# Kernel optimization log

Hardware: AMD Instinct MI355X
Metric: run time of the kernel (lower is better)

Reference implementation:

```python
import jax, jax.numpy as jnp
import numpy as np

N_NODES = 10000
N_EDGES = 200000
NODE_DIM = 128
EDGE_DIM = 16
CONV_DIM = 64
HEADS = 5
NEG_SLOPE = 0.2


def gatv2_layer(x, src, dst, edge_attr, Wl, bl, We, att, bias):
    # PyG GATv2Conv, share_weights=True, concat=False, add_self_loops=True, eval mode
    N = x.shape[0]
    H, C = att.shape
    xl = (x @ Wl + bl).reshape(N, H, C)  # [N,H,C]; x_r = x_l (share_weights)
    # self loops, edge_attr fill_value='mean' (mean of incoming edge_attr per node)
    deg = jax.ops.segment_sum(jnp.ones(dst.shape[0], x.dtype), dst, num_segments=N)
    loop_attr = jax.ops.segment_sum(edge_attr, dst, num_segments=N) / jnp.maximum(deg, 1.0)[:, None]
    loop = jnp.arange(N, dtype=src.dtype)
    src_f = jnp.concatenate([src, loop])
    dst_f = jnp.concatenate([dst, loop])
    ea = jnp.concatenate([edge_attr, loop_attr], axis=0)
    e_emb = (ea @ We).reshape(-1, H, C)  # [E+N,H,C]
    m = jax.nn.leaky_relu(xl[src_f] + xl[dst_f] + e_emb, NEG_SLOPE)
    score = jnp.einsum('ehc,hc->eh', m, att)  # [E+N,H]
    # per-destination softmax over incoming edges
    smax = jax.ops.segment_max(score, dst_f, num_segments=N)
    ex = jnp.exp(score - smax[dst_f])
    denom = jax.ops.segment_sum(ex, dst_f, num_segments=N)
    alpha = ex / denom[dst_f]
    out = jax.ops.segment_sum(alpha[:, :, None] * xl[src_f], dst_f, num_segments=N)
    return out.mean(axis=1) + bias  # concat=False -> mean over heads


def setup_inputs() -> dict:
    key = jax.random.key(0)
    ks = jax.random.split(key, 32)
    inp = {
        'x': jax.random.normal(ks[0], (N_NODES, NODE_DIM), jnp.float32),
        'edge_index': jax.random.randint(ks[1], (2, N_EDGES), 0, N_NODES, dtype=jnp.int32),
        'edge_attr': jax.random.normal(ks[2], (N_EDGES, EDGE_DIM), jnp.float32),
    }
    in_dims = [NODE_DIM, CONV_DIM, CONV_DIM]
    HC = HEADS * CONV_DIM
    k = 3
    for l in range(3):
        d = in_dims[l]
        inp[f'Wl{l}'] = jax.random.normal(ks[k], (d, HC), jnp.float32) / np.float32(np.sqrt(d)); k += 1
        inp[f'bl{l}'] = jnp.zeros((HC,), jnp.float32)
        inp[f'We{l}'] = jax.random.normal(ks[k], (EDGE_DIM, HC), jnp.float32) / np.float32(np.sqrt(EDGE_DIM)); k += 1
        inp[f'att{l}'] = jax.random.normal(ks[k], (HEADS, CONV_DIM), jnp.float32) / np.float32(np.sqrt(CONV_DIM)); k += 1
        inp[f'b{l}'] = jnp.zeros((CONV_DIM,), jnp.float32)
    return inp


def reference(x, edge_index, edge_attr,
              Wl0, bl0, We0, att0, b0,
              Wl1, bl1, We1, att1, b1,
              Wl2, bl2, We2, att2, b2):
    src, dst = edge_index[0], edge_index[1]
    h = x
    layers = [(Wl0, bl0, We0, att0, b0), (Wl1, bl1, We1, att1, b1), (Wl2, bl2, We2, att2, b2)]
    for Wl, bl, We, att, b in layers:
        h = gatv2_layer(h, src, dst, edge_attr, Wl, bl, We, att, b)
        h = jax.nn.elu(h)
    return h
```

## Files before the change

### kernel.cpp

```cpp
#include <hip/hip_runtime.h>
#include <hip/hip_bf16.h>


#define NN 10000
#define NE 200000
#define ND 128
#define ED 16
#define CD 64
#define NH 5
#define HC 320
#define EF 210000
#define EFP 210048
#define NEG 0.2f
#define PB 824
#define TOTB 4120
#define PERX 515

typedef float f2 __attribute__((ext_vector_type(2)));

__global__ void k_count(const int* __restrict__ dst, int* __restrict__ deg) {
  int e = blockIdx.x * blockDim.x + threadIdx.x;
  if (e >= NE) return;
  atomicAdd(&deg[dst[e]], 1);
}

__global__ __launch_bounds__(1024) void k_scan(const int* __restrict__ deg,
                                               int* __restrict__ rowptr) {
  __shared__ int part[1024];
  int t = threadIdx.x;
  int base = t * 10;
  int local[10];
  int s = 0;
  #pragma unroll
  for (int j = 0; j < 10; j++) {
    int i = base + j;
    local[j] = (i < NN) ? deg[i] : 0;
    s += local[j];
  }
  part[t] = s;
  __syncthreads();
  for (int off = 1; off < 1024; off <<= 1) {
    int v = (t >= off) ? part[t - off] : 0;
    __syncthreads();
    part[t] += v;
    __syncthreads();
  }
  int prefix = (t > 0) ? part[t - 1] : 0;
  #pragma unroll
  for (int j = 0; j < 10; j++) {
    int i = base + j;
    if (i < NN) rowptr[i] = prefix;
    prefix += local[j];
  }
  if (t == 1023) rowptr[NN] = prefix;
}

__global__ void k_fill(const int* __restrict__ ei, const int* __restrict__ rowptr,
                       int* __restrict__ cursor, int* __restrict__ csr_eid,
                       int* __restrict__ csr_src, int* __restrict__ csr_dst) {
  int e = blockIdx.x * blockDim.x + threadIdx.x;
  if (e >= NE) return;
  int d = ei[NE + e];
  int slot = atomicAdd(&cursor[d], 1);
  int pos = rowptr[d] + slot;
  csr_eid[pos] = e;
  csr_src[pos] = ei[e];
  csr_dst[pos] = d;
}

__global__ void k_eacsr(const int* __restrict__ csr_eid, const float* __restrict__ eattr,
                        float* __restrict__ ea_csr) {
  int idx = blockIdx.x * blockDim.x + threadIdx.x;
  if (idx >= NE * 4) return;
  int p = idx >> 2, q = idx & 3;
  const float4* sp = (const float4*)(eattr + (size_t)csr_eid[p] * ED);
  ((float4*)(ea_csr + (size_t)p * ED))[q] = sp[q];
}

__global__ __launch_bounds__(256) void k_loopattr(const float* __restrict__ ea_csr,
                                                  const int* __restrict__ rowptr,
                                                  float* __restrict__ loop_attr) {
  int wave = threadIdx.x >> 6, lane = threadIdx.x & 63;
  int d = blockIdx.x * 4 + wave;
  if (d >= NN) return;
  int g = lane >> 4, k = lane & 15;
  int b = rowptr[d], n = rowptr[d + 1] - b;
  float s = 0.f;
  for (int i = g; i < n; i += 4)
    s += ea_csr[(size_t)(b + i) * ED + k];
  s += __shfl_xor(s, 16, 64);
  s += __shfl_xor(s, 32, 64);
  if (g == 0) loop_attr[d * ED + k] = s / fmaxf((float)n, 1.0f);
}

__global__ void k_wet3(const float* __restrict__ We0, const float* __restrict__ We1,
                       const float* __restrict__ We2, float* __restrict__ Wpk) {
  int i = blockIdx.x * blockDim.x + threadIdx.x;
  if (i >= 3 * ED * HC) return;
  int l = i / (ED * HC);
  int r = i - l * (ED * HC);
  const float* We = (l == 0) ? We0 : (l == 1) ? We1 : We2;
  int j  = r & 1;
  int k  = (r >> 1) & 15;
  int cp = (r >> 5) & 31;
  int h  = r >> 10;
  Wpk[i] = We[k * HC + h * CD + cp * 2 + j];
}

template <int D>
__global__ __launch_bounds__(320) void k_xl(const float* __restrict__ h,
                                            const float* __restrict__ Wl,
                                            const float* __restrict__ bl,
                                            float* __restrict__ xl) {
  constexpr int NPB = 8;
  int node0 = blockIdx.x * NPB;
  int t = threadIdx.x;
  float acc[NPB];
  #pragma unroll
  for (int i = 0; i < NPB; i++) acc[i] = 0.f;
  for (int k = 0; k < D; k += 4) {
    float w0 = Wl[(k + 0) * HC + t];
    float w1 = Wl[(k + 1) * HC + t];
    float w2 = Wl[(k + 2) * HC + t];
    float w3 = Wl[(k + 3) * HC + t];
    #pragma unroll
    for (int i = 0; i < NPB; i++) {
      float4 hv = *(const float4*)(h + (size_t)(node0 + i) * D + k);
      acc[i] += hv.x * w0 + hv.y * w1 + hv.z * w2 + hv.w * w3;
    }
  }
  float bv = bl[t];
  #pragma unroll
  for (int i = 0; i < NPB; i++)
    xl[(size_t)(node0 + i) * HC + t] = acc[i] + bv;
}

__global__ __launch_bounds__(256) void k_score(
    const int* __restrict__ csr_src, const int* __restrict__ csr_dst,
    const float* __restrict__ ea_csr, const float* __restrict__ loop_attr,
    const float* __restrict__ xl, const float* __restrict__ Wpk,
    const float* __restrict__ att, float* __restrict__ wP) {
  int bid = blockIdx.x;
  int w = (bid & 7) * PERX + (bid >> 3);
  int h = w / PB;
  int lb = w - h * PB;
  int p = lb * 256 + threadIdx.x;
  if (p >= EF) return;
  int s, d;
  const float* ea;
  if (p < NE) { s = csr_src[p]; d = csr_dst[p]; ea = ea_csr + (size_t)p * ED; }
  else        { s = d = p - NE; ea = loop_attr + (size_t)(p - NE) * ED; }
  float eas[16];
  {
    const float4* q = (const float4*)ea;
    float4 t0 = q[0], t1 = q[1], t2 = q[2], t3 = q[3];
    eas[0] = t0.x;  eas[1] = t0.y;  eas[2] = t0.z;  eas[3] = t0.w;
    eas[4] = t1.x;  eas[5] = t1.y;  eas[6] = t1.z;  eas[7] = t1.w;
    eas[8] = t2.x;  eas[9] = t2.y;  eas[10] = t2.z; eas[11] = t2.w;
    eas[12] = t3.x; eas[13] = t3.y; eas[14] = t3.z; eas[15] = t3.w;
  }
  const float* xsrow = xl + (size_t)s * HC + h * CD;
  const float* xdrow = xl + (size_t)d * HC + h * CD;
  const f2* wp = (const f2*)Wpk + (size_t)h * (CD / 2) * ED;
  const f2* ap = (const f2*)(att + (size_t)h * CD);
  f2 sc2 = {0.f, 0.f};
  const f2 zero = {0.f, 0.f};
  #pragma unroll 4
  for (int cb = 0; cb < CD; cb += 4) {
    int cp = cb >> 1;
    float4 xs4 = *(const float4*)(xsrow + cb);
    float4 xd4 = *(const float4*)(xdrow + cb);
    const f2* w0 = wp + (size_t)cp * ED;
    const f2* w1 = w0 + ED;
    f2 z0 = f2{xs4.x, xs4.y} + f2{xd4.x, xd4.y};
    f2 z1 = f2{xs4.z, xs4.w} + f2{xd4.z, xd4.w};
    #pragma unroll
    for (int k = 0; k < ED; k++) {
      z0 += w0[k] * eas[k];
      z1 += w1[k] * eas[k];
    }
    z0 = __builtin_elementwise_max(z0, zero) + NEG * __builtin_elementwise_min(z0, zero);
    z1 = __builtin_elementwise_max(z1, zero) + NEG * __builtin_elementwise_min(z1, zero);
    sc2 += z0 * ap[cp];
    sc2 += z1 * ap[cp + 1];
  }
  float sc = sc2.x + sc2.y;
  sc = fminf(fmaxf(sc, -60.f), 60.f);
  wP[(size_t)h * EFP + p] = __expf(sc);
}

__global__ __launch_bounds__(320) void k_agg(
    const int* __restrict__ csr_src, const int* __restrict__ rowptr,
    const float* __restrict__ wP, const float* __restrict__ xl,
    const float* __restrict__ bias, float* __restrict__ out) {
  __shared__ float s_v[NH][CD];
  int h = threadIdx.x >> 6, lane = threadIdx.x & 63;
  int d = blockIdx.x;
  int b = rowptr[d], pe = rowptr[d + 1];
  const float* sp = wP + (size_t)h * EFP;
  const float* xlh = xl + h * CD + lane;
  float dn = sp[NE + d];
  float acc = dn * xlh[(size_t)d * HC];
  int p = b;
  for (; p + 8 <= pe; p += 8) {
    int s0 = csr_src[p + 0], s1 = csr_src[p + 1];
    int s2 = csr_src[p + 2], s3 = csr_src[p + 3];
    int s4 = csr_src[p + 4], s5 = csr_src[p + 5];
    int s6 = csr_src[p + 6], s7 = csr_src[p + 7];
    float w0 = sp[p + 0], w1 = sp[p + 1], w2 = sp[p + 2], w3 = sp[p + 3];
    float w4 = sp[p + 4], w5 = sp[p + 5], w6 = sp[p + 6], w7 = sp[p + 7];
    float x0 = xlh[(size_t)s0 * HC];
    float x1 = xlh[(size_t)s1 * HC];
    float x2 = xlh[(size_t)s2 * HC];
    float x3 = xlh[(size_t)s3 * HC];
    float x4 = xlh[(size_t)s4 * HC];
    float x5 = xlh[(size_t)s5 * HC];
    float x6 = xlh[(size_t)s6 * HC];
    float x7 = xlh[(size_t)s7 * HC];
    dn += ((w0 + w1) + (w2 + w3)) + ((w4 + w5) + (w6 + w7));
    acc += ((w0 * x0 + w1 * x1) + (w2 * x2 + w3 * x3)) +
           ((w4 * x4 + w5 * x5) + (w6 * x6 + w7 * x7));
  }
  for (; p + 4 <= pe; p += 4) {
    int s0 = csr_src[p + 0], s1 = csr_src[p + 1];
    int s2 = csr_src[p + 2], s3 = csr_src[p + 3];
    float w0 = sp[p + 0], w1 = sp[p + 1], w2 = sp[p + 2], w3 = sp[p + 3];
    float x0 = xlh[(size_t)s0 * HC];
    float x1 = xlh[(size_t)s1 * HC];
    float x2 = xlh[(size_t)s2 * HC];
    float x3 = xlh[(size_t)s3 * HC];
    dn += (w0 + w1) + (w2 + w3);
    acc += (w0 * x0 + w1 * x1) + (w2 * x2 + w3 * x3);
  }
  for (; p < pe; p++) {
    int s0 = csr_src[p];
    float w0 = sp[p];
    dn += w0;
    acc += w0 * xlh[(size_t)s0 * HC];
  }
  s_v[h][lane] = acc / dn;
  __syncthreads();
  if (h == 0) {
    float v = s_v[0][lane] + s_v[1][lane] + s_v[2][lane] + s_v[3][lane] + s_v[4][lane];
    v = v * (1.0f / NH) + bias[lane];
    v = v > 0.f ? v : expm1f(v);
    out[(size_t)d * CD + lane] = v;
  }
}

static inline size_t aln(size_t x) { return (x + 255) & ~(size_t)255; }

extern "C" void kernel_launch(void* const* d_in, const int* in_sizes, int n_in,
                              void* d_out, int out_size, void* d_ws, size_t ws_size,
                              hipStream_t stream) {
  const float* x = (const float*)d_in[0];
  const int* ei = (const int*)d_in[1];
  const float* eattr = (const float*)d_in[2];

  char* w = (char*)d_ws;
  int* degi      = (int*)w;                 w += aln(NN * 4);
  int* cursor    = (int*)w;                 w += aln(NN * 4);
  int* rowptr    = (int*)w;                 w += aln((NN + 1) * 4);
  int* csr_eid   = (int*)w;                 w += aln((size_t)NE * 4);
  int* csr_src   = (int*)w;                 w += aln((size_t)NE * 4);
  int* csr_dst   = (int*)w;                 w += aln((size_t)NE * 4);
  float* loop_attr = (float*)w;             w += aln((size_t)NN * ED * 4);
  float* ea_csr  = (float*)w;               w += aln((size_t)NE * ED * 4);
  float* xl      = (float*)w;               w += aln((size_t)NN * HC * 4);
  float* wPbuf   = (float*)w;               w += aln((size_t)NH * EFP * 4);
  float* Wpk     = (float*)w;               w += aln((size_t)3 * ED * HC * 4);
  float* hbuf    = (float*)w;               w += aln((size_t)NN * CD * 4);

  hipMemsetAsync(degi, 0, NN * 4, stream);
  hipMemsetAsync(cursor, 0, NN * 4, stream);
  k_count<<<(NE + 255) / 256, 256, 0, stream>>>(ei + NE, degi);
  k_scan<<<1, 1024, 0, stream>>>(degi, rowptr);
  k_fill<<<(NE + 255) / 256, 256, 0, stream>>>(ei, rowptr, cursor, csr_eid, csr_src, csr_dst);
  k_eacsr<<<(NE * 4 + 255) / 256, 256, 0, stream>>>(csr_eid, eattr, ea_csr);
  k_loopattr<<<(NN + 3) / 4, 256, 0, stream>>>(ea_csr, rowptr, loop_attr);
  k_wet3<<<(3 * ED * HC + 255) / 256, 256, 0, stream>>>(
      (const float*)d_in[5], (const float*)d_in[10], (const float*)d_in[15], Wpk);

  for (int l = 0; l < 3; l++) {
    const float* Wl  = (const float*)d_in[3 + 5 * l];
    const float* bl  = (const float*)d_in[4 + 5 * l];
    const float* att = (const float*)d_in[6 + 5 * l];
    const float* b   = (const float*)d_in[7 + 5 * l];

    if (l == 0) k_xl<ND><<<NN / 8, 320, 0, stream>>>(x, Wl, bl, xl);
    else        k_xl<CD><<<NN / 8, 320, 0, stream>>>(hbuf, Wl, bl, xl);

    k_score<<<TOTB, 256, 0, stream>>>(csr_src, csr_dst, ea_csr, loop_attr,
                                      xl, Wpk + (size_t)l * ED * HC, att, wPbuf);

    float* dst_out = (l < 2) ? hbuf : (float*)d_out;
    k_agg<<<NN, 320, 0, stream>>>(csr_src, rowptr, wPbuf, xl, b, dst_out);
  }
}
```

Before: 461.6 us.

## Split aggregation per head with atomics, fuse edge-attr gather with loop-attr mean

The aggregation kernel now assigns one wave per (head, destination) pair across smaller 256-thread blocks with an XCD-aware block swizzle. Per-head results are combined with atomicAdd into an accumulator held in the output buffer, and a separate combine kernel applies the head mean, bias and ELU and re-zeroes the accumulator. The edge-attr CSR gather is fused into the loop-attr mean kernel, and the two memsets are merged into one. This aims to improve load balance and occupancy in aggregation and drop one launch and one pass over edge attributes, at the cost of float atomics (nondeterministic summation order) and an extra launch per layer.

```diff
diff --git a/kernel.cpp b/kernel.cpp
--- a/kernel.cpp
+++ b/kernel.cpp
@@ -15,6 +15,9 @@
 #define PB 824
 #define TOTB 4120
 #define PERX 515
+#define NW_AGG 50000
+#define BL_AGG 12504
+#define PERXA 1563
 
 typedef float f2 __attribute__((ext_vector_type(2)));
 
@@ -68,26 +71,22 @@
   csr_dst[pos] = d;
 }
 
-__global__ void k_eacsr(const int* __restrict__ csr_eid, const float* __restrict__ eattr,
-                        float* __restrict__ ea_csr) {
-  int idx = blockIdx.x * blockDim.x + threadIdx.x;
-  if (idx >= NE * 4) return;
-  int p = idx >> 2, q = idx & 3;
-  const float4* sp = (const float4*)(eattr + (size_t)csr_eid[p] * ED);
-  ((float4*)(ea_csr + (size_t)p * ED))[q] = sp[q];
-}
-
-__global__ __launch_bounds__(256) void k_loopattr(const float* __restrict__ ea_csr,
-                                                  const int* __restrict__ rowptr,
-                                                  float* __restrict__ loop_attr) {
+__global__ __launch_bounds__(256) void k_eal(const int* __restrict__ csr_eid,
+                                             const float* __restrict__ eattr,
+                                             const int* __restrict__ rowptr,
+                                             float* __restrict__ ea_csr,
+                                             float* __restrict__ loop_attr) {
   int wave = threadIdx.x >> 6, lane = threadIdx.x & 63;
   int d = blockIdx.x * 4 + wave;
   if (d >= NN) return;
   int g = lane >> 4, k = lane & 15;
   int b = rowptr[d], n = rowptr[d + 1] - b;
   float s = 0.f;
-  for (int i = g; i < n; i += 4)
-    s += ea_csr[(size_t)(b + i) * ED + k];
+  for (int i = g; i < n; i += 4) {
+    float v = eattr[(size_t)csr_eid[b + i] * ED + k];
+    ea_csr[(size_t)(b + i) * ED + k] = v;
+    s += v;
+  }
   s += __shfl_xor(s, 16, 64);
   s += __shfl_xor(s, 32, 64);
   if (g == 0) loop_attr[d * ED + k] = s / fmaxf((float)n, 1.0f);
@@ -189,13 +188,17 @@
   wP[(size_t)h * EFP + p] = __expf(sc);
 }
 
-__global__ __launch_bounds__(320) void k_agg(
+__global__ __launch_bounds__(256) void k_agg2(
     const int* __restrict__ csr_src, const int* __restrict__ rowptr,
     const float* __restrict__ wP, const float* __restrict__ xl,
-    const float* __restrict__ bias, float* __restrict__ out) {
-  __shared__ float s_v[NH][CD];
-  int h = threadIdx.x >> 6, lane = threadIdx.x & 63;
-  int d = blockIdx.x;
+    float* __restrict__ accum) {
+  int bid = blockIdx.x;
+  int b2 = (bid & 7) * PERXA + (bid >> 3);
+  int wv = threadIdx.x >> 6, lane = threadIdx.x & 63;
+  int g = b2 * 4 + wv;
+  if (g >= NW_AGG) return;
+  int h = g / NN;
+  int d = g - h * NN;
   int b = rowptr[d], pe = rowptr[d + 1];
   const float* sp = wP + (size_t)h * EFP;
   const float* xlh = xl + h * CD + lane;
@@ -238,14 +241,20 @@
     dn += w0;
     acc += w0 * xlh[(size_t)s0 * HC];
   }
-  s_v[h][lane] = acc / dn;
-  __syncthreads();
-  if (h == 0) {
-    float v = s_v[0][lane] + s_v[1][lane] + s_v[2][lane] + s_v[3][lane] + s_v[4][lane];
-    v = v * (1.0f / NH) + bias[lane];
-    v = v > 0.f ? v : expm1f(v);
-    out[(size_t)d * CD + lane] = v;
-  }
+  atomicAdd(&accum[(size_t)d * CD + lane], acc / dn);
+}
+
+__global__ __launch_bounds__(256) void k_comb(float* accum,
+                                              const float* __restrict__ bias,
+                                              float* out) {
+  int idx = blockIdx.x * blockDim.x + threadIdx.x;
+  if (idx >= NN * CD) return;
+  int c = idx & (CD - 1);
+  float v = accum[idx];
+  accum[idx] = 0.f;
+  v = v * (1.0f / NH) + bias[c];
+  v = v > 0.f ? v : expm1f(v);
+  out[idx] = v;
 }
 
 static inline size_t aln(size_t x) { return (x + 255) & ~(size_t)255; }
@@ -270,14 +279,14 @@
   float* wPbuf   = (float*)w;               w += aln((size_t)NH * EFP * 4);
   float* Wpk     = (float*)w;               w += aln((size_t)3 * ED * HC * 4);
   float* hbuf    = (float*)w;               w += aln((size_t)NN * CD * 4);
-
-  hipMemsetAsync(degi, 0, NN * 4, stream);
-  hipMemsetAsync(cursor, 0, NN * 4, stream);
+  float* accum   = (float*)d_out;
+
+  hipMemsetAsync(degi, 0, 2 * aln(NN * 4), stream);
+  hipMemsetAsync(accum, 0, (size_t)NN * CD * 4, stream);
   k_count<<<(NE + 255) / 256, 256, 0, stream>>>(ei + NE, degi);
   k_scan<<<1, 1024, 0, stream>>>(degi, rowptr);
   k_fill<<<(NE + 255) / 256, 256, 0, stream>>>(ei, rowptr, cursor, csr_eid, csr_src, csr_dst);
-  k_eacsr<<<(NE * 4 + 255) / 256, 256, 0, stream>>>(csr_eid, eattr, ea_csr);
-  k_loopattr<<<(NN + 3) / 4, 256, 0, stream>>>(ea_csr, rowptr, loop_attr);
+  k_eal<<<(NN + 3) / 4, 256, 0, stream>>>(csr_eid, eattr, rowptr, ea_csr, loop_attr);
   k_wet3<<<(3 * ED * HC + 255) / 256, 256, 0, stream>>>(
       (const float*)d_in[5], (const float*)d_in[10], (const float*)d_in[15], Wpk);
 
@@ -293,7 +302,9 @@
     k_score<<<TOTB, 256, 0, stream>>>(csr_src, csr_dst, ea_csr, loop_attr,
                                       xl, Wpk + (size_t)l * ED * HC, att, wPbuf);
 
+    k_agg2<<<BL_AGG, 256, 0, stream>>>(csr_src, rowptr, wPbuf, xl, accum);
+
     float* dst_out = (l < 2) ? hbuf : (float*)d_out;
-    k_agg<<<NN, 320, 0, stream>>>(csr_src, rowptr, wPbuf, xl, b, dst_out);
-  }
-}
+    k_comb<<<(NN * CD + 255) / 256, 256, 0, stream>>>(accum, b, dst_out);
+  }
+}
```

Result: no change. 469.6 us (+1.7%).
